# Optimization experiments

Measured on AMD Instinct MI355X. Metric: run time of the kernel, lower is better.

The kernel has to match this reference:

```python
import jax, jax.numpy as jnp
import numpy as np

PATCH_SIZE = 128
NUM_HEADS = 16
DILATION = 1
POS_BND = int(0.8 * PATCH_SIZE * DILATION ** 0.5)  # 102
RPE_NUM = 2 * POS_BND + 1                            # 205
B, P = 256, PATCH_SIZE


def setup_inputs() -> dict:
    key = jax.random.key(0)
    k1, k2 = jax.random.split(key)
    # relative integer coordinates, roughly centered at 0 (clamped inside reference)
    xyz = jax.random.randint(k1, (B, P, P, 3), -150, 151, dtype=jnp.int32).astype(jnp.int64)
    # trunc_normal_(std=0.02) approximated by scaled normal
    rpe_table = jax.random.normal(k2, (3 * RPE_NUM, NUM_HEADS), dtype=jnp.float32) * 0.02
    return {"xyz": xyz, "rpe_table": rpe_table}


def reference(xyz, rpe_table):
    # idx: clamp coords, shift to [0, 2*pos_bnd], offset each axis into its table slice
    mul = jnp.arange(3, dtype=xyz.dtype) * RPE_NUM              # [3]
    idx = jnp.clip(xyz, -POS_BND, POS_BND) + POS_BND + mul      # [B,P,P,3]
    out = rpe_table[idx]                                        # [B,P,P,3,H] gather
    out = out.sum(axis=3)                                       # [B,P,P,H] sum over xyz axes
    return out.transpose(0, 3, 1, 2)                            # [B,H,P,P]
```

## Files before the change

### kernel.cpp

```cpp
#include <hip/hip_runtime.h>
#include <hip/hip_bf16.h>

#define P 128
#define NH 16
#define POS_BND 102
#define RPE_NUM 205
#define TROWS (3 * RPE_NUM)
#define TSTRIDE 12
#define SWS 68
#define ROWS_PER_BLOCK 16

typedef float floatx4 __attribute__((ext_vector_type(4)));

__device__ __forceinline__ float blo(unsigned d) { return __uint_as_float(d << 16); }
__device__ __forceinline__ float bhi(unsigned d) { return __uint_as_float(d & 0xffff0000u); }

__global__ __launch_bounds__(256)
void rpe_kernel(const int* __restrict__ xyz, const float* __restrict__ table,
                float* __restrict__ out) {
    __shared__ unsigned lt[TROWS * TSTRIDE];
    __shared__ float sw[4][8][SWS];

    const int t = threadIdx.x;
    const int w = t >> 6;
    const int l = t & 63;

    for (int q = t; q < TROWS * 8; q += 256) {
        int row = q >> 3, d = q & 7;
        float2 v = reinterpret_cast<const float2*>(table)[row * 8 + d];
        unsigned a = (__float_as_uint(v.x) + 0x8000u) >> 16;
        unsigned b = (__float_as_uint(v.y) + 0x8000u) & 0xffff0000u;
        lt[row * TSTRIDE + d] = a | b;
    }
    __syncthreads();

    const int r0 = blockIdx.x * ROWS_PER_BLOCK;

    int x0, x1, x2;
    {
        const int* xp = xyz + (((size_t)(r0 + 4 * w) * P) + l) * 3;
        x0 = xp[0]; x1 = xp[1]; x2 = xp[2];
    }

    for (int k = 0; k < 8; ++k) {
        const int r  = r0 + 4 * w + (k >> 1);
        const int jh = k & 1;
        const int b  = r >> 7;
        const int i  = r & 127;

        int y0 = x0, y1 = x1, y2 = x2;
        if (k < 7) {
            const int rn = r0 + 4 * w + ((k + 1) >> 1);
            const int jn = ((k + 1) & 1) * 64;
            const int* xp = xyz + (((size_t)rn * P) + jn + l) * 3;
            x0 = xp[0]; x1 = xp[1]; x2 = xp[2];
        }

        const int i0 = min(max(y0, -POS_BND), POS_BND) + POS_BND;
        const int i1 = min(max(y1, -POS_BND), POS_BND) + POS_BND + RPE_NUM;
        const int i2 = min(max(y2, -POS_BND), POS_BND) + POS_BND + 2 * RPE_NUM;

        const size_t obase = (((size_t)b * NH) * P + i) * P + (size_t)(jh * 64);
        float* swp = &sw[w][0][l];

        #pragma unroll
        for (int hh = 0; hh < 2; ++hh) {
            uint4 ga = *reinterpret_cast<const uint4*>(&lt[i0 * TSTRIDE + hh * 4]);
            uint4 gb = *reinterpret_cast<const uint4*>(&lt[i1 * TSTRIDE + hh * 4]);
            uint4 gc = *reinterpret_cast<const uint4*>(&lt[i2 * TSTRIDE + hh * 4]);

            swp[0*SWS] = blo(ga.x) + blo(gb.x) + blo(gc.x);
            swp[1*SWS] = bhi(ga.x) + bhi(gb.x) + bhi(gc.x);
            swp[2*SWS] = blo(ga.y) + blo(gb.y) + blo(gc.y);
            swp[3*SWS] = bhi(ga.y) + bhi(gb.y) + bhi(gc.y);
            swp[4*SWS] = blo(ga.z) + blo(gb.z) + blo(gc.z);
            swp[5*SWS] = bhi(ga.z) + bhi(gb.z) + bhi(gc.z);
            swp[6*SWS] = blo(ga.w) + blo(gb.w) + blo(gc.w);
            swp[7*SWS] = bhi(ga.w) + bhi(gb.w) + bhi(gc.w);

            #pragma unroll
            for (int it = 0; it < 2; ++it) {
                int hl = it * 4 + (l >> 4);
                int j4 = l & 15;
                floatx4 v = *reinterpret_cast<const floatx4*>(&sw[w][hl][j4 * 4]);
                size_t o = obase + (size_t)(hh * 8 + hl) * (P * P) + (size_t)(j4 * 4);
                __builtin_nontemporal_store(v, reinterpret_cast<floatx4*>(out + o));
            }
        }
    }
}

extern "C" void kernel_launch(void* const* d_in, const int* in_sizes, int n_in,
                              void* d_out, int out_size, void* d_ws, size_t ws_size,
                              hipStream_t stream) {
    const int*   xyz   = (const int*)d_in[0];
    const float* table = (const float*)d_in[1];
    float*       out   = (float*)d_out;

    const int total_rows = 256 * P;
    const int grid = total_rows / ROWS_PER_BLOCK;
    rpe_kernel<<<grid, 256, 0, stream>>>(xyz, table, out);
}
```

Measured before the change: 57.64 us.

## Process two j-lanes per thread with split-half LDS table and bf16 staging

```diff
diff --git a/kernel.cpp b/kernel.cpp
--- a/kernel.cpp
+++ b/kernel.cpp
@@ -5,87 +5,116 @@
 #define NH 16
 #define POS_BND 102
 #define RPE_NUM 205
-#define TROWS (3 * RPE_NUM)
-#define TSTRIDE 12
-#define SWS 68
+#define TROWS 615
+#define HALF_OFF 2460
 #define ROWS_PER_BLOCK 16
 
 typedef float floatx4 __attribute__((ext_vector_type(4)));
 
 __device__ __forceinline__ float blo(unsigned d) { return __uint_as_float(d << 16); }
 __device__ __forceinline__ float bhi(unsigned d) { return __uint_as_float(d & 0xffff0000u); }
+__device__ __forceinline__ unsigned pkbf(float a, float b) {
+    unsigned r;
+    asm("v_cvt_pk_bf16_f32 %0, %1, %2" : "=v"(r) : "v"(a), "v"(b));
+    return r;
+}
 
-__global__ __launch_bounds__(256)
+__global__ __launch_bounds__(256, 3)
 void rpe_kernel(const int* __restrict__ xyz, const float* __restrict__ table,
                 float* __restrict__ out) {
-    __shared__ unsigned lt[TROWS * TSTRIDE];
-    __shared__ float sw[4][8][SWS];
+    __shared__ unsigned lt[2 * HALF_OFF];
+    __shared__ unsigned su[4][NH][128];
 
     const int t = threadIdx.x;
-    const int w = t >> 6;
-    const int l = t & 63;
+    const int w = t >> 6, l = t & 63;
 
     for (int q = t; q < TROWS * 8; q += 256) {
         int row = q >> 3, d = q & 7;
         float2 v = reinterpret_cast<const float2*>(table)[row * 8 + d];
         unsigned a = (__float_as_uint(v.x) + 0x8000u) >> 16;
         unsigned b = (__float_as_uint(v.y) + 0x8000u) & 0xffff0000u;
-        lt[row * TSTRIDE + d] = a | b;
+        int dst = (d < 4) ? (row * 4 + d) : (HALF_OFF + row * 4 + (d - 4));
+        lt[dst] = a | b;
+    }
+
+    const int r0 = blockIdx.x * ROWS_PER_BLOCK + 4 * w;
+    const int2* xp = reinterpret_cast<const int2*>(xyz);
+
+    int2 p0, p1, p2, p3, p4, p5;
+    {
+        size_t ba = (size_t)192 * r0 + 3 * l;
+        size_t bb = (size_t)192 * (r0 + 1) + 3 * l;
+        p0 = xp[ba]; p1 = xp[ba + 1]; p2 = xp[ba + 2];
+        p3 = xp[bb]; p4 = xp[bb + 1]; p5 = xp[bb + 2];
     }
     __syncthreads();
 
-    const int r0 = blockIdx.x * ROWS_PER_BLOCK;
+    #pragma unroll
+    for (int k = 0; k < 2; ++k) {
+        const int ra = r0 + 2 * k;
+        const int b  = ra >> 7;
+        const int i  = ra & 127;
 
-    int x0, x1, x2;
-    {
-        const int* xp = xyz + (((size_t)(r0 + 4 * w) * P) + l) * 3;
-        x0 = xp[0]; x1 = xp[1]; x2 = xp[2];
-    }
-
-    for (int k = 0; k < 8; ++k) {
-        const int r  = r0 + 4 * w + (k >> 1);
-        const int jh = k & 1;
-        const int b  = r >> 7;
-        const int i  = r & 127;
-
-        int y0 = x0, y1 = x1, y2 = x2;
-        if (k < 7) {
-            const int rn = r0 + 4 * w + ((k + 1) >> 1);
-            const int jn = ((k + 1) & 1) * 64;
-            const int* xp = xyz + (((size_t)rn * P) + jn + l) * 3;
-            x0 = xp[0]; x1 = xp[1]; x2 = xp[2];
+        int2 c0 = p0, c1 = p1, c2 = p2, c3 = p3, c4 = p4, c5 = p5;
+        if (k == 0) {
+            size_t ba = (size_t)192 * (r0 + 2) + 3 * l;
+            size_t bb = (size_t)192 * (r0 + 3) + 3 * l;
+            p0 = xp[ba]; p1 = xp[ba + 1]; p2 = xp[ba + 2];
+            p3 = xp[bb]; p4 = xp[bb + 1]; p5 = xp[bb + 2];
         }
 
-        const int i0 = min(max(y0, -POS_BND), POS_BND) + POS_BND;
-        const int i1 = min(max(y1, -POS_BND), POS_BND) + POS_BND + RPE_NUM;
-        const int i2 = min(max(y2, -POS_BND), POS_BND) + POS_BND + 2 * RPE_NUM;
+        #pragma unroll
+        for (int s = 0; s < 2; ++s) {
+            int x0, y0, z0, x1, y1, z1;
+            if (s == 0) { x0 = c0.x; y0 = c0.y; z0 = c1.x; x1 = c1.y; y1 = c2.x; z1 = c2.y; }
+            else        { x0 = c3.x; y0 = c3.y; z0 = c4.x; x1 = c4.y; y1 = c5.x; z1 = c5.y; }
 
-        const size_t obase = (((size_t)b * NH) * P + i) * P + (size_t)(jh * 64);
-        float* swp = &sw[w][0][l];
+            int t00 = min(max(x0, -POS_BND), POS_BND) + POS_BND;
+            int t01 = min(max(y0, -POS_BND), POS_BND) + POS_BND + RPE_NUM;
+            int t02 = min(max(z0, -POS_BND), POS_BND) + POS_BND + 2 * RPE_NUM;
+            int t10 = min(max(x1, -POS_BND), POS_BND) + POS_BND;
+            int t11 = min(max(y1, -POS_BND), POS_BND) + POS_BND + RPE_NUM;
+            int t12 = min(max(z1, -POS_BND), POS_BND) + POS_BND + 2 * RPE_NUM;
 
+            uint4 ga0 = *reinterpret_cast<const uint4*>(&lt[t00 * 4]);
+            uint4 ga1 = *reinterpret_cast<const uint4*>(&lt[t01 * 4]);
+            uint4 ga2 = *reinterpret_cast<const uint4*>(&lt[t02 * 4]);
+            uint4 gb0 = *reinterpret_cast<const uint4*>(&lt[HALF_OFF + t00 * 4]);
+            uint4 gb1 = *reinterpret_cast<const uint4*>(&lt[HALF_OFF + t01 * 4]);
+            uint4 gb2 = *reinterpret_cast<const uint4*>(&lt[HALF_OFF + t02 * 4]);
+            uint4 gc0 = *reinterpret_cast<const uint4*>(&lt[t10 * 4]);
+            uint4 gc1 = *reinterpret_cast<const uint4*>(&lt[t11 * 4]);
+            uint4 gc2 = *reinterpret_cast<const uint4*>(&lt[t12 * 4]);
+            uint4 gd0 = *reinterpret_cast<const uint4*>(&lt[HALF_OFF + t10 * 4]);
+            uint4 gd1 = *reinterpret_cast<const uint4*>(&lt[HALF_OFF + t11 * 4]);
+            uint4 gd2 = *reinterpret_cast<const uint4*>(&lt[HALF_OFF + t12 * 4]);
+
+            unsigned* srow = &su[w][0][s * 64 + l];
+            srow[ 0*128] = pkbf(blo(ga0.x)+blo(ga1.x)+blo(ga2.x), blo(gc0.x)+blo(gc1.x)+blo(gc2.x));
+            srow[ 1*128] = pkbf(bhi(ga0.x)+bhi(ga1.x)+bhi(ga2.x), bhi(gc0.x)+bhi(gc1.x)+bhi(gc2.x));
+            srow[ 2*128] = pkbf(blo(ga0.y)+blo(ga1.y)+blo(ga2.y), blo(gc0.y)+blo(gc1.y)+blo(gc2.y));
+            srow[ 3*128] = pkbf(bhi(ga0.y)+bhi(ga1.y)+bhi(ga2.y), bhi(gc0.y)+bhi(gc1.y)+bhi(gc2.y));
+            srow[ 4*128] = pkbf(blo(ga0.z)+blo(ga1.z)+blo(ga2.z), blo(gc0.z)+blo(gc1.z)+blo(gc2.z));
+            srow[ 5*128] = pkbf(bhi(ga0.z)+bhi(ga1.z)+bhi(ga2.z), bhi(gc0.z)+bhi(gc1.z)+bhi(gc2.z));
+            srow[ 6*128] = pkbf(blo(ga0.w)+blo(ga1.w)+blo(ga2.w), blo(gc0.w)+blo(gc1.w)+blo(gc2.w));
+            srow[ 7*128] = pkbf(bhi(ga0.w)+bhi(ga1.w)+bhi(ga2.w), bhi(gc0.w)+bhi(gc1.w)+bhi(gc2.w));
+            srow[ 8*128] = pkbf(blo(gb0.x)+blo(gb1.x)+blo(gb2.x), blo(gd0.x)+blo(gd1.x)+blo(gd2.x));
+            srow[ 9*128] = pkbf(bhi(gb0.x)+bhi(gb1.x)+bhi(gb2.x), bhi(gd0.x)+bhi(gd1.x)+bhi(gd2.x));
+            srow[10*128] = pkbf(blo(gb0.y)+blo(gb1.y)+blo(gb2.y), blo(gd0.y)+blo(gd1.y)+blo(gd2.y));
+            srow[11*128] = pkbf(bhi(gb0.y)+bhi(gb1.y)+bhi(gb2.y), bhi(gd0.y)+bhi(gd1.y)+bhi(gd2.y));
+            srow[12*128] = pkbf(blo(gb0.z)+blo(gb1.z)+blo(gb2.z), blo(gd0.z)+blo(gd1.z)+blo(gd2.z));
+            srow[13*128] = pkbf(bhi(gb0.z)+bhi(gb1.z)+bhi(gb2.z), bhi(gd0.z)+bhi(gd1.z)+bhi(gd2.z));
+            srow[14*128] = pkbf(blo(gb0.w)+blo(gb1.w)+blo(gb2.w), blo(gd0.w)+blo(gd1.w)+blo(gd2.w));
+            srow[15*128] = pkbf(bhi(gb0.w)+bhi(gb1.w)+bhi(gb2.w), bhi(gd0.w)+bhi(gd1.w)+bhi(gd2.w));
+        }
+
+        const size_t pbase = ((size_t)b * NH) * (P * P) + (size_t)i * P + 4 * l;
         #pragma unroll
-        for (int hh = 0; hh < 2; ++hh) {
-            uint4 ga = *reinterpret_cast<const uint4*>(&lt[i0 * TSTRIDE + hh * 4]);
-            uint4 gb = *reinterpret_cast<const uint4*>(&lt[i1 * TSTRIDE + hh * 4]);
-            uint4 gc = *reinterpret_cast<const uint4*>(&lt[i2 * TSTRIDE + hh * 4]);
-
-            swp[0*SWS] = blo(ga.x) + blo(gb.x) + blo(gc.x);
-            swp[1*SWS] = bhi(ga.x) + bhi(gb.x) + bhi(gc.x);
-            swp[2*SWS] = blo(ga.y) + blo(gb.y) + blo(gc.y);
-            swp[3*SWS] = bhi(ga.y) + bhi(gb.y) + bhi(gc.y);
-            swp[4*SWS] = blo(ga.z) + blo(gb.z) + blo(gc.z);
-            swp[5*SWS] = bhi(ga.z) + bhi(gb.z) + bhi(gc.z);
-            swp[6*SWS] = blo(ga.w) + blo(gb.w) + blo(gc.w);
-            swp[7*SWS] = bhi(ga.w) + bhi(gb.w) + bhi(gc.w);
-
-            #pragma unroll
-            for (int it = 0; it < 2; ++it) {
-                int hl = it * 4 + (l >> 4);
-                int j4 = l & 15;
-                floatx4 v = *reinterpret_cast<const floatx4*>(&sw[w][hl][j4 * 4]);
-                size_t o = obase + (size_t)(hh * 8 + hl) * (P * P) + (size_t)(j4 * 4);
-                __builtin_nontemporal_store(v, reinterpret_cast<floatx4*>(out + o));
-            }
+        for (int h = 0; h < NH; ++h) {
+            uint2 v = *reinterpret_cast<const uint2*>(&su[w][h][2 * l]);
+            floatx4 f = { blo(v.x), bhi(v.x), blo(v.y), bhi(v.y) };
+            __builtin_nontemporal_store(f,
+                reinterpret_cast<floatx4*>(out + pbase + (size_t)h * (P * P)));
         }
     }
 }
```

Measured after the change: 54.89 us. 1.05x faster.
